# Kernel optimization log

Hardware: AMD Instinct MI355X
Metric: run time of the kernel (lower is better)

## Reference

```python
import jax, jax.numpy as jnp
import numpy as np

B, N, D, H = 64, 196, 768, 3072
QMAX = 127.0  # 8-bit symmetric: clamp to [-128, 127]


def ste_round(x):
    # straight-through-estimator round (QAT)
    return x + jax.lax.stop_gradient(jnp.round(x) - x)


def q_linear_diag(x, w, b, a_sf):
    """Quantized diagonal linear (ResMLP Affine / LayerScale as QuantLinear)."""
    w_sf = jnp.max(jnp.abs(w)) / QMAX            # per-tensor weight scale
    w_int = ste_round(w / w_sf)                  # int8 weights (|.|<=127)
    out_int = (x / a_sf) * w_int
    if b is not None:
        out_int = out_int + ste_round(b / (a_sf * w_sf))  # 32-bit bias
    return out_int * (a_sf * w_sf), w_sf


def q_linear_dense(x, w, b, a_sf):
    """Quantized dense linear: int8 GEMM + int32 bias, dequant with a_sf*w_sf."""
    w_sf = jnp.max(jnp.abs(w)) / QMAX
    w_int = jnp.clip(ste_round(w / w_sf), -QMAX - 1, QMAX)
    out_int = jnp.einsum('...i,oi->...o', x / a_sf, w_int) + ste_round(b / (a_sf * w_sf))
    return out_int * (a_sf * w_sf), w_sf


def q_act(x, pre_sf, new_sf, identity=None, id_sf=None):
    """HAWQ-style QuantAct: fixed-point requantization to scale new_sf (8-bit)."""
    if identity is None:
        z_int = ste_round(x / pre_sf)
        out_int = ste_round(z_int * (pre_sf / new_sf))
    else:
        # main branch (x - identity) requantized with pre_sf, identity with id_sf
        z_int = ste_round((x - identity) / pre_sf)
        out_int = ste_round(z_int * (pre_sf / new_sf)) \
                + ste_round(ste_round(identity / id_sf) * (id_sf / new_sf))
    out_int = jnp.clip(out_int, -QMAX - 1, QMAX)
    return out_int * new_sf, new_sf


def _forward(x, norm1_w, norm1_b, attn_w, attn_b, gamma1_w,
             norm2_w, norm2_b, fc1_w, fc1_b, fc2_w, fc2_b, gamma2_w, act_sfs):
    a_sf = act_sfs[0]
    # --- token-mixing half ---
    identity, id_sf = x, a_sf
    x, w_sf = q_linear_diag(x, norm1_w, norm1_b, a_sf)         # norm1 (affine)
    x = jnp.swapaxes(x, 1, 2)                                  # [B, D, N]
    x, a_sf = q_act(x, a_sf * w_sf, act_sfs[1])                # quant_act1
    x, w_sf = q_linear_dense(x, attn_w, attn_b, a_sf)          # attn (cross-patch)
    x = jnp.swapaxes(x, 1, 2)                                  # [B, N, D]
    x, a_sf = q_act(x, a_sf * w_sf, act_sfs[2])                # quant_act2
    x, w_sf = q_linear_diag(x, gamma1_w, None, a_sf)           # gamma_1 (layerscale)
    x = x + identity
    x, a_sf = q_act(x, a_sf * w_sf, act_sfs[3], identity, id_sf)  # quant_act_int32_1
    # --- MLP half ---
    identity, id_sf = x, a_sf
    x, w_sf = q_linear_diag(x, norm2_w, norm2_b, a_sf)         # norm2
    x, a_sf = q_act(x, a_sf * w_sf, act_sfs[4])                # quant_act3
    x, w_sf = q_linear_dense(x, fc1_w, fc1_b, a_sf)            # mlp.fc1
    x = jax.nn.relu(x)
    x, a_sf = q_act(x, a_sf * w_sf, act_sfs[5])                # mlp.quant_act1
    x, w_sf = q_linear_dense(x, fc2_w, fc2_b, a_sf)            # mlp.fc2
    x, a_sf = q_act(x, a_sf * w_sf, act_sfs[6])                # mlp.quant_act2
    x, w_sf = q_linear_diag(x, gamma2_w, None, a_sf)           # gamma_2
    x = x + identity
    x, a_sf = q_act(x, a_sf * w_sf, act_sfs[7], identity, id_sf)  # quant_act_int32_2
    return x, a_sf


def setup_inputs() -> dict:
    key = jax.random.key(0)
    ks = jax.random.split(key, 16)
    act_sfs = jax.random.uniform(ks[14], (8,), jnp.float32, 0.02, 0.06)
    x = jax.random.normal(ks[0], (B, N, D), jnp.float32)
    # input is already quantized at scale act_sfs[0]
    x = jnp.clip(jnp.round(x / act_sfs[0]), -128, 127) * act_sfs[0]
    s = 0.05
    return {
        'x': x,
        'norm1_w': 1.0 + s * jax.random.normal(ks[1], (D,), jnp.float32),
        'norm1_b': s * jax.random.normal(ks[2], (D,), jnp.float32),
        'attn_w': jax.random.normal(ks[3], (N, N), jnp.float32) / np.sqrt(N),
        'attn_b': s * jax.random.normal(ks[4], (N,), jnp.float32),
        'gamma1_w': 0.1 + s * jax.random.normal(ks[5], (D,), jnp.float32),
        'norm2_w': 1.0 + s * jax.random.normal(ks[6], (D,), jnp.float32),
        'norm2_b': s * jax.random.normal(ks[7], (D,), jnp.float32),
        'fc1_w': jax.random.normal(ks[8], (H, D), jnp.float32) / np.sqrt(D),
        'fc1_b': s * jax.random.normal(ks[9], (H,), jnp.float32),
        'fc2_w': jax.random.normal(ks[10], (D, H), jnp.float32) / np.sqrt(H),
        'fc2_b': s * jax.random.normal(ks[11], (D,), jnp.float32),
        'gamma2_w': 0.1 + s * jax.random.normal(ks[12], (D,), jnp.float32),
        'act_sfs': act_sfs,
    }


def reference(x, norm1_w, norm1_b, attn_w, attn_b, gamma1_w,
              norm2_w, norm2_b, fc1_w, fc1_b, fc2_w, fc2_b, gamma2_w, act_sfs):
    return _forward(x, norm1_w, norm1_b, attn_w, attn_b, gamma1_w,
                    norm2_w, norm2_b, fc1_w, fc1_b, fc2_w, fc2_b, gamma2_w, act_sfs)
```

## Files before the change

kernel.cpp:

```cpp
#include <hip/hip_runtime.h>

#define B_ 64
#define N_ 196
#define D_ 768
#define H_ 3072
#define M_ (B_*N_)
#define NP 256

typedef int int4v __attribute__((ext_vector_type(4)));
typedef signed char i8;

#define WS_MAX 0
#define WS_W1F 16
#define WS_B1F (16+768)
#define WS_G1F (16+768*2)
#define WS_W2F (16+768*3)
#define WS_B2F (16+768*4)
#define WS_G2F (16+768*5)
#define WS_BA  (16+768*6)
#define WS_BF1 (WS_BA+256)
#define WS_BF2 (WS_BF1+3072)
#define OFF_WA   40960ull
#define OFF_FC1  (OFF_WA+65536ull)
#define OFF_FC2  (OFF_FC1+2359296ull)
#define OFF_X2   (OFF_FC2+2359296ull)
#define OFF_Q3   (OFF_X2+9633792ull)
#define OFF_Q4   (OFF_Q3+9633792ull)
#define OFF_Q1T  OFF_Q4

__device__ __forceinline__ float clamp8(float v){ return fminf(fmaxf(v,-128.f),127.f); }

__device__ __forceinline__ void async16(const void* g, void* l){
    __builtin_amdgcn_global_load_lds((const __attribute__((address_space(1))) void*)g,
                                     (__attribute__((address_space(3))) void*)l, 16, 0, 0);
}

__global__ void k_init(char* ws, const float* __restrict__ act, float* out_tail){
    int id = blockIdx.x*256 + threadIdx.x;
    if (blockIdx.x == 0){
        float* f = (float*)ws;
        if (threadIdx.x < 8) f[WS_MAX+threadIdx.x] = 0.f;
        if (threadIdx.x == 8) *out_tail = act[7];
    }
    if (id < 4096){ int4v z = {0,0,0,0}; ((int4v*)(ws+OFF_WA))[id] = z; }
}

__global__ void k_maxabs(const float* __restrict__ p0, const float* __restrict__ p1,
                         const float* __restrict__ p2, const float* __restrict__ p3,
                         const float* __restrict__ p4, const float* __restrict__ p5,
                         const float* __restrict__ p6, float* wsmax){
    const float* ps[7] = {p0,p1,p2,p3,p4,p5,p6};
    const int    n4s[7] = {192, 9604, 192, 192, 589824, 589824, 192};
    int tid = blockIdx.y;
    const float4* p = (const float4*)ps[tid]; int n4 = n4s[tid];
    float m = 0.f;
    for (int i = blockIdx.x*blockDim.x + threadIdx.x; i < n4; i += gridDim.x*blockDim.x){
        float4 v = p[i];
        m = fmaxf(m, fmaxf(fmaxf(fabsf(v.x),fabsf(v.y)), fmaxf(fabsf(v.z),fabsf(v.w))));
    }
    #pragma unroll
    for (int off = 32; off; off >>= 1) m = fmaxf(m, __shfl_down(m, off, 64));
    __shared__ float red[4];
    int lane = threadIdx.x & 63, wv = threadIdx.x >> 6;
    if (lane == 0) red[wv] = m;
    __syncthreads();
    if (threadIdx.x == 0){
        float mm = red[0];
        for (int w = 1; w < (int)blockDim.x/64; w++) mm = fmaxf(mm, red[w]);
        atomicMax((unsigned*)&wsmax[tid], __float_as_uint(mm));
    }
}

__device__ __forceinline__ size_t frag_off(int o, int k, int K){
    int g = o >> 4, c = k >> 6;
    int lane = (o & 15) + (((k >> 4) & 3) << 4);
    return (((size_t)g*(K>>6) + c)*64 + lane)*16 + (k & 15);
}

__global__ void k_qweights(const float* __restrict__ n1w, const float* __restrict__ n1b,
                           const float* __restrict__ aw,  const float* __restrict__ ab,
                           const float* __restrict__ g1w, const float* __restrict__ n2w,
                           const float* __restrict__ n2b, const float* __restrict__ f1w,
                           const float* __restrict__ f1b, const float* __restrict__ f2w,
                           const float* __restrict__ f2b, const float* __restrict__ g2w,
                           const float* __restrict__ act, char* ws){
    float* fws = (float*)ws;
    int*   iws = (int*)ws;
    const float* mx = fws + WS_MAX;
    long i = (long)blockIdx.x*blockDim.x + threadIdx.x;
    const long F4 = 589824;
    if (i < F4){ float sf = mx[4]/127.0f;
        float4 v = ((const float4*)f1w)[i];
        int o = (int)(i/192), kb = (int)(i%192)*4;
        unsigned b0 = (unsigned)(unsigned char)(i8)(int)fminf(fmaxf(rintf(v.x/sf),-128.f),127.f);
        unsigned b1 = (unsigned)(unsigned char)(i8)(int)fminf(fmaxf(rintf(v.y/sf),-128.f),127.f);
        unsigned b2 = (unsigned)(unsigned char)(i8)(int)fminf(fmaxf(rintf(v.z/sf),-128.f),127.f);
        unsigned b3 = (unsigned)(unsigned char)(i8)(int)fminf(fmaxf(rintf(v.w/sf),-128.f),127.f);
        *(unsigned*)(ws + OFF_FC1 + frag_off(o, kb, 768)) = b0 | (b1<<8) | (b2<<16) | (b3<<24);
        return; }
    i -= F4;
    if (i < F4){ float sf = mx[5]/127.0f;
        float4 v = ((const float4*)f2w)[i];
        int o = (int)(i/768), kb = (int)(i%768)*4;
        unsigned b0 = (unsigned)(unsigned char)(i8)(int)fminf(fmaxf(rintf(v.x/sf),-128.f),127.f);
        unsigned b1 = (unsigned)(unsigned char)(i8)(int)fminf(fmaxf(rintf(v.y/sf),-128.f),127.f);
        unsigned b2 = (unsigned)(unsigned char)(i8)(int)fminf(fmaxf(rintf(v.z/sf),-128.f),127.f);
        unsigned b3 = (unsigned)(unsigned char)(i8)(int)fminf(fmaxf(rintf(v.w/sf),-128.f),127.f);
        *(unsigned*)(ws + OFF_FC2 + frag_off(o, kb, 3072)) = b0 | (b1<<8) | (b2<<16) | (b3<<24);
        return; }
    i -= F4;
    if (i < 38416){ float sf = mx[1]/127.0f;
        int o = (int)(i/196), k = (int)(i%196);
        ((i8*)(ws+OFF_WA))[frag_off(o, k, NP)] =
            (i8)(int)fminf(fmaxf(rintf(aw[i]/sf),-128.f),127.f); return; }
    i -= 38416;
    if (i < 768){ float sf = mx[0]/127.0f; fws[WS_W1F+i] = rintf(n1w[i]/sf); return; }
    i -= 768;
    if (i < 768){ float sf = mx[0]/127.0f; fws[WS_B1F+i] = rintf(n1b[i]/(act[0]*sf)); return; }
    i -= 768;
    if (i < 768){ float sf = mx[2]/127.0f; fws[WS_G1F+i] = rintf(g1w[i]/sf); return; }
    i -= 768;
    if (i < 768){ float sf = mx[3]/127.0f; fws[WS_W2F+i] = rintf(n2w[i]/sf); return; }
    i -= 768;
    if (i < 768){ float sf = mx[3]/127.0f; fws[WS_B2F+i] = rintf(n2b[i]/(act[3]*sf)); return; }
    i -= 768;
    if (i < 768){ float sf = mx[6]/127.0f; fws[WS_G2F+i] = rintf(g2w[i]/sf); return; }
    i -= 768;
    if (i < 196){ float sf = mx[1]/127.0f; iws[WS_BA+i] = (int)rintf(ab[i]/(act[1]*sf)); return; }
    i -= 196;
    if (i < 3072){ float sf = mx[4]/127.0f; iws[WS_BF1+i] = (int)rintf(f1b[i]/(act[4]*sf)); return; }
    i -= 3072;
    if (i < 768){ float sf = mx[5]/127.0f; iws[WS_BF2+i] = (int)rintf(f2b[i]/(act[5]*sf)); return; }
}

__global__ __launch_bounds__(256) void k_stage1(const float* __restrict__ x,
                                                const char* __restrict__ wsc,
                                                char* __restrict__ ws,
                                                const float* __restrict__ act){
    __shared__ i8 T[64][80];
    const float* fws = (const float*)wsc;
    int b = blockIdx.z, n0 = blockIdx.y*64, d0 = blockIdx.x*64;
    int t = threadIdx.x;
    float a0 = act[0];
    float w1sf = fws[WS_MAX+0]/127.0f;
    float r1 = (a0*w1sf)/act[1];
    int dl = (t & 15) * 4;
    int d  = d0 + dl;
    float4 wv = *(const float4*)(fws + WS_W1F + d);
    float4 bv = *(const float4*)(fws + WS_B1F + d);
    #pragma unroll
    for (int pass = 0; pass < 4; pass++){
        int nl = (t >> 4) + pass*16;
        int n  = n0 + nl;
        i8 q[4] = {0,0,0,0};
        if (n < 196){
            float4 xv = *(const float4*)(x + ((size_t)b*196 + n)*768 + d);
            float o0 = rintf(xv.x/a0*wv.x + bv.x);
            float o1 = rintf(xv.y/a0*wv.y + bv.y);
            float o2 = rintf(xv.z/a0*wv.z + bv.z);
            float o3 = rintf(xv.w/a0*wv.w + bv.w);
            q[0] = (i8)(int)clamp8(rintf(o0*r1));
            q[1] = (i8)(int)clamp8(rintf(o1*r1));
            q[2] = (i8)(int)clamp8(rintf(o2*r1));
            q[3] = (i8)(int)clamp8(rintf(o3*r1));
        }
        T[dl+0][nl] = q[0]; T[dl+1][nl] = q[1];
        T[dl+2][nl] = q[2]; T[dl+3][nl] = q[3];
    }
    __syncthreads();
    i8* q1T = (i8*)(ws + OFF_Q1T) + (size_t)b*(48*4*1024);
    int gl = t >> 6, lane = t & 63;
    int d_loc = gl*16 + (lane & 15);
    int n16   = ((lane >> 4) & 3) * 16;
    int4v v = *(const int4v*)&T[d_loc][n16];
    size_t dst = (((size_t)((d0>>4)+gl)*4 + (n0>>6))*64 + lane)*16;
    *(int4v*)(q1T + dst) = v;
}

__device__ __forceinline__ void gemm_i8_bd(const i8* __restrict__ qa, const i8* __restrict__ wbF,
                                           size_t lda, int n0, int K, int4v acc[4][4],
                                           i8* As, int t){
    int lane = t & 63;
    int w = t >> 6, wm = w & 1, wn = w >> 1;
    int lr = lane >> 2, lc = lane & 3;
    const i8* ga = qa + (size_t)(w*32 + lr)*lda + lc*16;
    int loff = (w*32 + lr)*64 + lc*16;
    int kc = K >> 6;
    size_t ntS = (size_t)kc*1024;
    const i8* gb = wbF + ((size_t)((n0>>4) + wn*4))*ntS + lane*16;
    int arow = (wm*64 + (lane&15))*64 + (lane>>4)*16;
    int4v a[4], b0[4], b1[4];
    async16(ga,          As + loff);
    async16(ga + 16*lda, As + loff + 16*64);
    #pragma unroll
    for (int nt=0;nt<4;nt++) b0[nt] = *(const int4v*)(gb + nt*ntS);
    for (int i = 0; i < kc; i += 2){
        __syncthreads();
        if (i+1 < kc){
            async16(ga + (i+1)*64,          As + 8192 + loff);
            async16(ga + (i+1)*64 + 16*lda, As + 8192 + loff + 16*64);
            #pragma unroll
            for (int nt=0;nt<4;nt++) b1[nt] = *(const int4v*)(gb + (i+1)*1024 + nt*ntS);
        }
        #pragma unroll
        for (int mt=0;mt<4;mt++) a[mt] = *(const int4v*)(As + arow + mt*1024);
        #pragma unroll
        for (int mt=0;mt<4;mt++)
            #pragma unroll
            for (int nt=0;nt<4;nt++)
                acc[mt][nt] = __builtin_amdgcn_mfma_i32_16x16x64_i8(a[mt], b0[nt], acc[mt][nt],0,0,0);
        __syncthreads();
        if (i+2 < kc){
            async16(ga + (i+2)*64,          As + loff);
            async16(ga + (i+2)*64 + 16*lda, As + loff + 16*64);
            #pragma unroll
            for (int nt=0;nt<4;nt++) b0[nt] = *(const int4v*)(gb + (i+2)*1024 + nt*ntS);
        }
        #pragma unroll
        for (int mt=0;mt<4;mt++) a[mt] = *(const int4v*)(As + 8192 + arow + mt*1024);
        #pragma unroll
        for (int mt=0;mt<4;mt++)
            #pragma unroll
            for (int nt=0;nt<4;nt++)
                acc[mt][nt] = __builtin_amdgcn_mfma_i32_16x16x64_i8(a[mt], b1[nt], acc[mt][nt],0,0,0);
    }
}

__global__ __launch_bounds__(256) void k_attn(const char* __restrict__ ws,
                                              const float* __restrict__ x,
                                              const float* __restrict__ act){
    __shared__ char smem[32768];
    const float* fws = (const float*)ws;
    const int*   iws = (const int*)ws;
    int b = blockIdx.z;
    int m0 = blockIdx.x*128, n0 = blockIdx.y*128;
    int t = threadIdx.x, lane = t & 63;
    int wm = (t>>6)&1, wn = t>>7;
    const i8* pa = (const i8*)(ws + OFF_WA)  + ((size_t)((m0>>4)+wm*4)*4)*1024 + lane*16;
    const i8* pb = (const i8*)(ws + OFF_Q1T) + (size_t)b*(48*4*1024)
                   + ((size_t)((n0>>4)+wn*4)*4)*1024 + lane*16;
    int4v acc[4][4]; int4v zz = {0,0,0,0};
    #pragma unroll
    for (int mt=0;mt<4;mt++) for (int nt=0;nt<4;nt++) acc[mt][nt] = zz;
    int4v a0[4], b0[4], a1[4], b1[4];
    #pragma unroll
    for (int mt=0;mt<4;mt++) a0[mt] = *(const int4v*)(pa + mt*4096);
    #pragma unroll
    for (int nt=0;nt<4;nt++) b0[nt] = *(const int4v*)(pb + nt*4096);
    for (int c = 0; c < 4; c += 2){
        #pragma unroll
        for (int mt=0;mt<4;mt++) a1[mt] = *(const int4v*)(pa + (c+1)*1024 + mt*4096);
        #pragma unroll
        for (int nt=0;nt<4;nt++) b1[nt] = *(const int4v*)(pb + (c+1)*1024 + nt*4096);
        #pragma unroll
        for (int mt=0;mt<4;mt++)
            #pragma unroll
            for (int nt=0;nt<4;nt++)
                acc[mt][nt] = __builtin_amdgcn_mfma_i32_16x16x64_i8(a0[mt], b0[nt], acc[mt][nt],0,0,0);
        if (c+2 < 4){
            #pragma unroll
            for (int mt=0;mt<4;mt++) a0[mt] = *(const int4v*)(pa + (c+2)*1024 + mt*4096);
            #pragma unroll
            for (int nt=0;nt<4;nt++) b0[nt] = *(const int4v*)(pb + (c+2)*1024 + nt*4096);
        }
        #pragma unroll
        for (int mt=0;mt<4;mt++)
            #pragma unroll
            for (int nt=0;nt<4;nt++)
                acc[mt][nt] = __builtin_amdgcn_mfma_i32_16x16x64_i8(a1[mt], b1[nt], acc[mt][nt],0,0,0);
    }

    float a0s=act[0], a1s=act[1], a2=act[2], a3=act[3], a4=act[4];
    float wasf = fws[WS_MAX+1]/127.0f; float r2  = (a1s*wasf)/a2;
    float g1sf = fws[WS_MAX+2]/127.0f; float r3a = (a2*g1sf)/a3; float r3b = a0s/a3;
    float w2sf = fws[WS_MAX+3]/127.0f; float r4  = (a3*w2sf)/a4;
    float g1v[4], w2v[4], b2v[4];
    #pragma unroll
    for (int nt=0;nt<4;nt++){
        int d = n0 + wn*64 + nt*16 + (lane&15);
        g1v[nt] = fws[WS_G1F + d]; w2v[nt] = fws[WS_W2F + d]; b2v[nt] = fws[WS_B2F + d];
    }
    i8* Xs = (i8*)smem;
    i8* Qs = (i8*)smem + 16384;
    i8* x2 = (i8*)(ws + OFF_X2);
    i8* q3 = (i8*)(ws + OFF_Q3);
    #pragma unroll
    for (int mt=0;mt<4;mt++){
        #pragma unroll
        for (int r=0;r<4;r++){
            int ml = wm*64 + mt*16 + (lane>>4)*4 + r;
            int o  = m0 + ml;
            int ba = iws[WS_BA + o];
            #pragma unroll
            for (int nt=0;nt<4;nt++){
                int nl = wn*64 + nt*16 + (lane&15);
                int d  = n0 + nl;
                float s2 = (float)(acc[mt][nt][r] + ba);
                float q2 = clamp8(rintf(s2*r2));
                float o3v = q2*g1v[nt];
                float xv = (o < 196) ? x[((size_t)b*196 + o)*768 + d] : 0.f;
                float idi = rintf(xv/a0s);
                float tt = rintf(o3v*r3a) + rintf(idi*r3b);
                tt = clamp8(tt);
                float o4 = tt*w2v[nt] + b2v[nt];
                float qr = clamp8(rintf(o4*r4));
                Xs[ml*128 + nl] = (i8)(int)tt;
                Qs[ml*128 + nl] = (i8)(int)qr;
            }
        }
    }
    __syncthreads();
    #pragma unroll
    for (int e=0;e<4;e++){
        int id = t + e*256;
        int row = id>>3, c = id&7;
        int o = m0 + row;
        if (o < 196){
            size_t g = ((size_t)b*196 + o)*768 + n0 + c*16;
            *(int4v*)(x2 + g) = *(const int4v*)(Xs + row*128 + c*16);
            *(int4v*)(q3 + g) = *(const int4v*)(Qs + row*128 + c*16);
        }
    }
}

__global__ __launch_bounds__(256) void k_fc1(const char* __restrict__ ws, const float* __restrict__ act){
    __shared__ char smem[16384];
    const float* fws = (const float*)ws;
    const int*   iws = (const int*)ws;
    int m0 = blockIdx.x*128, n0 = blockIdx.y*128;
    const i8* qa = (const i8*)(ws+OFF_Q3) + (size_t)m0*768;
    const i8* wb = (const i8*)(ws+OFF_FC1);
    const int* bias = iws + WS_BF1;
    i8* qout = (i8*)(ws+OFF_Q4);
    int t = threadIdx.x, lane = t & 63;
    int wm = (t>>6)&1, wn = t>>7;
    int4v acc[4][4]; int4v zz = {0,0,0,0};
    #pragma unroll
    for (int mt=0;mt<4;mt++) for (int nt=0;nt<4;nt++) acc[mt][nt] = zz;
    gemm_i8_bd(qa, wb, 768, n0, 768, acc, (i8*)smem, t);
    float wsf = fws[WS_MAX+4]/127.0f;
    float r5 = (act[4]*wsf)/act[5];
    int bcol[4];
    #pragma unroll
    for (int nt=0;nt<4;nt++) bcol[nt] = bias[n0 + wn*64 + nt*16 + (lane&15)];
    __syncthreads();
    i8* Cs = (i8*)smem;
    #pragma unroll
    for (int mt=0;mt<4;mt++){
        #pragma unroll
        for (int nt=0;nt<4;nt++){
            int nl = wn*64 + nt*16 + (lane&15);
            #pragma unroll
            for (int r=0;r<4;r++){
                int s = acc[mt][nt][r] + bcol[nt];
                if (s < 0) s = 0;
                float q = clamp8(rintf((float)s * r5));
                int ml = wm*64 + mt*16 + (lane>>4)*4 + r;
                Cs[ml*128 + nl] = (i8)(int)q;
            }
        }
    }
    __syncthreads();
    #pragma unroll
    for (int e=0;e<4;e++){
        int id2 = t + e*256;
        int row = id2>>3, c = id2&7;
        *(int4v*)(qout + (size_t)(m0+row)*3072 + n0 + c*16) = *(const int4v*)(Cs + row*128 + c*16);
    }
}

__global__ __launch_bounds__(256) void k_fc2(const char* __restrict__ ws, const float* __restrict__ act,
                                             float* __restrict__ out){
    __shared__ char smem[16384];
    const float* fws = (const float*)ws;
    const int*   iws = (const int*)ws;
    int m0 = blockIdx.x*128, n0 = blockIdx.y*128;
    const i8* qa = (const i8*)(ws+OFF_Q4) + (size_t)m0*3072;
    const i8* wb = (const i8*)(ws+OFF_FC2);
    const int* bias = iws + WS_BF2;
    const float* g2f = fws + WS_G2F;
    const i8* x2 = (const i8*)(ws+OFF_X2);
    int t = threadIdx.x, lane = t & 63;
    int wm = (t>>6)&1, wn = t>>7;
    int4v acc[4][4]; int4v zz = {0,0,0,0};
    #pragma unroll
    for (int mt=0;mt<4;mt++) for (int nt=0;nt<4;nt++) acc[mt][nt] = zz;
    gemm_i8_bd(qa, wb, 3072, n0, 3072, acc, (i8*)smem, t);
    float a3=act[3], a5=act[5], a6=act[6], a7=act[7];
    float wsf  = fws[WS_MAX+5]/127.0f; float r6  = (a5*wsf)/a6;
    float g2sf = fws[WS_MAX+6]/127.0f; float r7a = (a6*g2sf)/a7; float r7b = a3/a7;
    int bcol[4]; float g2v[4];
    #pragma unroll
    for (int nt=0;nt<4;nt++){
        int nc = n0 + wn*64 + nt*16 + (lane&15);
        bcol[nt] = bias[nc]; g2v[nt] = g2f[nc];
    }
    #pragma unroll
    for (int mt=0;mt<4;mt++){
        #pragma unroll
        for (int nt=0;nt<4;nt++){
            int nc = n0 + wn*64 + nt*16 + (lane&15);
            #pragma unroll
            for (int r=0;r<4;r++){
                int ml = wm*64 + mt*16 + (lane>>4)*4 + r;
                size_t gi = (size_t)(m0+ml)*768 + nc;
                int s = acc[mt][nt][r] + bcol[nt];
                float q6 = clamp8(rintf((float)s*r6));
                float o7 = q6*g2v[nt];
                float idi = (float)x2[gi];
                float tt = rintf(o7*r7a) + rintf(idi*r7b);
                tt = clamp8(tt);
                out[gi] = tt*a7;
            }
        }
    }
}

extern "C" void kernel_launch(void* const* d_in, const int* in_sizes, int n_in,
                              void* d_out, int out_size, void* d_ws, size_t ws_size,
                              hipStream_t stream){
    const float* x   = (const float*)d_in[0];
    const float* n1w = (const float*)d_in[1];
    const float* n1b = (const float*)d_in[2];
    const float* aw  = (const float*)d_in[3];
    const float* ab  = (const float*)d_in[4];
    const float* g1w = (const float*)d_in[5];
    const float* n2w = (const float*)d_in[6];
    const float* n2b = (const float*)d_in[7];
    const float* f1w = (const float*)d_in[8];
    const float* f1b = (const float*)d_in[9];
    const float* f2w = (const float*)d_in[10];
    const float* f2b = (const float*)d_in[11];
    const float* g2w = (const float*)d_in[12];
    const float* act = (const float*)d_in[13];
    char* ws = (char*)d_ws;
    float* out = (float*)d_out;

    k_init<<<16,256,0,stream>>>(ws, act, out + (size_t)B_*N_*D_);
    k_maxabs<<<dim3(120,7),256,0,stream>>>(n1w, aw, g1w, n2w, f1w, f2w, g2w, (float*)ws);
    long qwThreads = 2L*589824 + 38416 + 768L*6 + 196 + 3072 + 768;
    k_qweights<<<(int)((qwThreads+255)/256),256,0,stream>>>(n1w,n1b,aw,ab,g1w,n2w,n2b,
                                                            f1w,f1b,f2w,f2b,g2w,act,ws);
    k_stage1<<<dim3(12,4,64),256,0,stream>>>(x, ws, ws, act);
    k_attn<<<dim3(2,6,64),256,0,stream>>>(ws, x, act);
    k_fc1<<<dim3(98,24),256,0,stream>>>(ws, act);
    k_fc2<<<dim3(98,6),256,0,stream>>>(ws, act, out);
}
```

Baseline: 299.4 us.

## Store fc1/fc2 activations in MFMA fragment layout and load directly to registers

The producer kernels (attn epilogue and fc1 epilogue) now write the quantized activations Q3 and Q4 in a pre-tiled MFMA fragment order instead of row-major. This lets fc1 and fc2 read both A and B operands straight from global memory into registers with a shared double-buffered helper, removing the LDS staging, async global-to-LDS copies and the per-step barriers. The trade-off is no LDS reuse of A tiles across waves, so each wave fetches its own A fragments from global/L2, and the epilogue scatter writes are more complex.

```diff
diff --git a/kernel.cpp b/kernel.cpp
--- a/kernel.cpp
+++ b/kernel.cpp
@@ -29,11 +29,6 @@
 #define OFF_Q1T  OFF_Q4
 
 __device__ __forceinline__ float clamp8(float v){ return fminf(fmaxf(v,-128.f),127.f); }
-
-__device__ __forceinline__ void async16(const void* g, void* l){
-    __builtin_amdgcn_global_load_lds((const __attribute__((address_space(1))) void*)g,
-                                     (__attribute__((address_space(3))) void*)l, 16, 0, 0);
-}
 
 __global__ void k_init(char* ws, const float* __restrict__ act, float* out_tail){
     int id = blockIdx.x*256 + threadIdx.x;
@@ -177,52 +172,35 @@
     *(int4v*)(q1T + dst) = v;
 }
 
-__device__ __forceinline__ void gemm_i8_bd(const i8* __restrict__ qa, const i8* __restrict__ wbF,
-                                           size_t lda, int n0, int K, int4v acc[4][4],
-                                           i8* As, int t){
-    int lane = t & 63;
-    int w = t >> 6, wm = w & 1, wn = w >> 1;
-    int lr = lane >> 2, lc = lane & 3;
-    const i8* ga = qa + (size_t)(w*32 + lr)*lda + lc*16;
-    int loff = (w*32 + lr)*64 + lc*16;
-    int kc = K >> 6;
-    size_t ntS = (size_t)kc*1024;
-    const i8* gb = wbF + ((size_t)((n0>>4) + wn*4))*ntS + lane*16;
-    int arow = (wm*64 + (lane&15))*64 + (lane>>4)*16;
-    int4v a[4], b0[4], b1[4];
-    async16(ga,          As + loff);
-    async16(ga + 16*lda, As + loff + 16*64);
-    #pragma unroll
-    for (int nt=0;nt<4;nt++) b0[nt] = *(const int4v*)(gb + nt*ntS);
-    for (int i = 0; i < kc; i += 2){
-        __syncthreads();
-        if (i+1 < kc){
-            async16(ga + (i+1)*64,          As + 8192 + loff);
-            async16(ga + (i+1)*64 + 16*lda, As + 8192 + loff + 16*64);
-            #pragma unroll
-            for (int nt=0;nt<4;nt++) b1[nt] = *(const int4v*)(gb + (i+1)*1024 + nt*ntS);
-        }
-        #pragma unroll
-        for (int mt=0;mt<4;mt++) a[mt] = *(const int4v*)(As + arow + mt*1024);
+__device__ __forceinline__ void gemm_i8_direct_frag(const i8* pa, const i8* pb,
+                                                    int KC, size_t sA, size_t sB,
+                                                    int4v acc[4][4]){
+    int4v a0[4], b0[4], a1[4], b1[4];
+    #pragma unroll
+    for (int mt=0;mt<4;mt++) a0[mt] = *(const int4v*)(pa + mt*sA);
+    #pragma unroll
+    for (int nt=0;nt<4;nt++) b0[nt] = *(const int4v*)(pb + nt*sB);
+    for (int c = 0; c < KC; c += 2){
+        #pragma unroll
+        for (int mt=0;mt<4;mt++) a1[mt] = *(const int4v*)(pa + (c+1)*1024 + mt*sA);
+        #pragma unroll
+        for (int nt=0;nt<4;nt++) b1[nt] = *(const int4v*)(pb + (c+1)*1024 + nt*sB);
         #pragma unroll
         for (int mt=0;mt<4;mt++)
             #pragma unroll
             for (int nt=0;nt<4;nt++)
-                acc[mt][nt] = __builtin_amdgcn_mfma_i32_16x16x64_i8(a[mt], b0[nt], acc[mt][nt],0,0,0);
-        __syncthreads();
-        if (i+2 < kc){
-            async16(ga + (i+2)*64,          As + loff);
-            async16(ga + (i+2)*64 + 16*lda, As + loff + 16*64);
-            #pragma unroll
-            for (int nt=0;nt<4;nt++) b0[nt] = *(const int4v*)(gb + (i+2)*1024 + nt*ntS);
-        }
-        #pragma unroll
-        for (int mt=0;mt<4;mt++) a[mt] = *(const int4v*)(As + 8192 + arow + mt*1024);
+                acc[mt][nt] = __builtin_amdgcn_mfma_i32_16x16x64_i8(a0[mt], b0[nt], acc[mt][nt],0,0,0);
+        if (c+2 < KC){
+            #pragma unroll
+            for (int mt=0;mt<4;mt++) a0[mt] = *(const int4v*)(pa + (c+2)*1024 + mt*sA);
+            #pragma unroll
+            for (int nt=0;nt<4;nt++) b0[nt] = *(const int4v*)(pb + (c+2)*1024 + nt*sB);
+        }
         #pragma unroll
         for (int mt=0;mt<4;mt++)
             #pragma unroll
             for (int nt=0;nt<4;nt++)
-                acc[mt][nt] = __builtin_amdgcn_mfma_i32_16x16x64_i8(a[mt], b1[nt], acc[mt][nt],0,0,0);
+                acc[mt][nt] = __builtin_amdgcn_mfma_i32_16x16x64_i8(a1[mt], b1[nt], acc[mt][nt],0,0,0);
     }
 }
 
@@ -242,33 +220,7 @@
     int4v acc[4][4]; int4v zz = {0,0,0,0};
     #pragma unroll
     for (int mt=0;mt<4;mt++) for (int nt=0;nt<4;nt++) acc[mt][nt] = zz;
-    int4v a0[4], b0[4], a1[4], b1[4];
-    #pragma unroll
-    for (int mt=0;mt<4;mt++) a0[mt] = *(const int4v*)(pa + mt*4096);
-    #pragma unroll
-    for (int nt=0;nt<4;nt++) b0[nt] = *(const int4v*)(pb + nt*4096);
-    for (int c = 0; c < 4; c += 2){
-        #pragma unroll
-        for (int mt=0;mt<4;mt++) a1[mt] = *(const int4v*)(pa + (c+1)*1024 + mt*4096);
-        #pragma unroll
-        for (int nt=0;nt<4;nt++) b1[nt] = *(const int4v*)(pb + (c+1)*1024 + nt*4096);
-        #pragma unroll
-        for (int mt=0;mt<4;mt++)
-            #pragma unroll
-            for (int nt=0;nt<4;nt++)
-                acc[mt][nt] = __builtin_amdgcn_mfma_i32_16x16x64_i8(a0[mt], b0[nt], acc[mt][nt],0,0,0);
-        if (c+2 < 4){
-            #pragma unroll
-            for (int mt=0;mt<4;mt++) a0[mt] = *(const int4v*)(pa + (c+2)*1024 + mt*4096);
-            #pragma unroll
-            for (int nt=0;nt<4;nt++) b0[nt] = *(const int4v*)(pb + (c+2)*1024 + nt*4096);
-        }
-        #pragma unroll
-        for (int mt=0;mt<4;mt++)
-            #pragma unroll
-            for (int nt=0;nt<4;nt++)
-                acc[mt][nt] = __builtin_amdgcn_mfma_i32_16x16x64_i8(a1[mt], b1[nt], acc[mt][nt],0,0,0);
-    }
+    gemm_i8_direct_frag(pa, pb, 4, 4096, 4096, acc);
 
     float a0s=act[0], a1s=act[1], a2=act[2], a3=act[3], a4=act[4];
     float wasf = fws[WS_MAX+1]/127.0f; float r2  = (a1s*wasf)/a2;
@@ -282,8 +234,8 @@
     }
     i8* Xs = (i8*)smem;
     i8* Qs = (i8*)smem + 16384;
-    i8* x2 = (i8*)(ws + OFF_X2);
-    i8* q3 = (i8*)(ws + OFF_Q3);
+    i8* x2  = (i8*)(ws + OFF_X2);
+    i8* q3F = (i8*)(ws + OFF_Q3);
     #pragma unroll
     for (int mt=0;mt<4;mt++){
         #pragma unroll
@@ -318,7 +270,11 @@
         if (o < 196){
             size_t g = ((size_t)b*196 + o)*768 + n0 + c*16;
             *(int4v*)(x2 + g) = *(const int4v*)(Xs + row*128 + c*16);
-            *(int4v*)(q3 + g) = *(const int4v*)(Qs + row*128 + c*16);
+            int r2i = b*196 + o;
+            int lane_d = (r2i & 15) + ((c & 3) << 4);
+            size_t dst = (((size_t)(r2i>>4))*12 + (size_t)(n0>>6) + (c>>2))*1024
+                         + (size_t)lane_d*16;
+            *(int4v*)(q3F + dst) = *(const int4v*)(Qs + row*128 + c*16);
         }
     }
 }
@@ -328,22 +284,21 @@
     const float* fws = (const float*)ws;
     const int*   iws = (const int*)ws;
     int m0 = blockIdx.x*128, n0 = blockIdx.y*128;
-    const i8* qa = (const i8*)(ws+OFF_Q3) + (size_t)m0*768;
-    const i8* wb = (const i8*)(ws+OFF_FC1);
-    const int* bias = iws + WS_BF1;
-    i8* qout = (i8*)(ws+OFF_Q4);
     int t = threadIdx.x, lane = t & 63;
     int wm = (t>>6)&1, wn = t>>7;
+    const i8* pa = (const i8*)(ws+OFF_Q3)  + ((size_t)(m0>>4) + wm*4)*(12*1024) + (size_t)lane*16;
+    const i8* pb = (const i8*)(ws+OFF_FC1) + ((size_t)(n0>>4) + wn*4)*(12*1024) + (size_t)lane*16;
+    const int* bias = iws + WS_BF1;
+    i8* q4F = (i8*)(ws+OFF_Q4);
     int4v acc[4][4]; int4v zz = {0,0,0,0};
     #pragma unroll
     for (int mt=0;mt<4;mt++) for (int nt=0;nt<4;nt++) acc[mt][nt] = zz;
-    gemm_i8_bd(qa, wb, 768, n0, 768, acc, (i8*)smem, t);
+    gemm_i8_direct_frag(pa, pb, 12, 12*1024, 12*1024, acc);
     float wsf = fws[WS_MAX+4]/127.0f;
     float r5 = (act[4]*wsf)/act[5];
     int bcol[4];
     #pragma unroll
     for (int nt=0;nt<4;nt++) bcol[nt] = bias[n0 + wn*64 + nt*16 + (lane&15)];
-    __syncthreads();
     i8* Cs = (i8*)smem;
     #pragma unroll
     for (int mt=0;mt<4;mt++){
@@ -363,29 +318,34 @@
     __syncthreads();
     #pragma unroll
     for (int e=0;e<4;e++){
-        int id2 = t + e*256;
-        int row = id2>>3, c = id2&7;
-        *(int4v*)(qout + (size_t)(m0+row)*3072 + n0 + c*16) = *(const int4v*)(Cs + row*128 + c*16);
+        int id = t + e*256;
+        int mg  = id >> 7;
+        int kc2 = (id >> 6) & 1;
+        int ld  = id & 63;
+        int row = mg*16 + (ld & 15);
+        int cb  = kc2*64 + ((ld>>4)&3)*16;
+        int4v v = *(const int4v*)(Cs + row*128 + cb);
+        size_t dst = (((size_t)(m0>>4) + mg)*48 + (size_t)(n0>>6) + kc2)*1024 + (size_t)ld*16;
+        *(int4v*)(q4F + dst) = v;
     }
 }
 
 __global__ __launch_bounds__(256) void k_fc2(const char* __restrict__ ws, const float* __restrict__ act,
                                              float* __restrict__ out){
-    __shared__ char smem[16384];
     const float* fws = (const float*)ws;
     const int*   iws = (const int*)ws;
     int m0 = blockIdx.x*128, n0 = blockIdx.y*128;
-    const i8* qa = (const i8*)(ws+OFF_Q4) + (size_t)m0*3072;
-    const i8* wb = (const i8*)(ws+OFF_FC2);
+    int t = threadIdx.x, lane = t & 63;
+    int wm = (t>>6)&1, wn = t>>7;
+    const i8* pa = (const i8*)(ws+OFF_Q4)  + ((size_t)(m0>>4) + wm*4)*(48*1024) + (size_t)lane*16;
+    const i8* pb = (const i8*)(ws+OFF_FC2) + ((size_t)(n0>>4) + wn*4)*(48*1024) + (size_t)lane*16;
     const int* bias = iws + WS_BF2;
     const float* g2f = fws + WS_G2F;
     const i8* x2 = (const i8*)(ws+OFF_X2);
-    int t = threadIdx.x, lane = t & 63;
-    int wm = (t>>6)&1, wn = t>>7;
     int4v acc[4][4]; int4v zz = {0,0,0,0};
     #pragma unroll
     for (int mt=0;mt<4;mt++) for (int nt=0;nt<4;nt++) acc[mt][nt] = zz;
-    gemm_i8_bd(qa, wb, 3072, n0, 3072, acc, (i8*)smem, t);
+    gemm_i8_direct_frag(pa, pb, 48, 48*1024, 48*1024, acc);
     float a3=act[3], a5=act[5], a6=act[6], a7=act[7];
     float wsf  = fws[WS_MAX+5]/127.0f; float r6  = (a5*wsf)/a6;
     float g2sf = fws[WS_MAX+6]/127.0f; float r7a = (a6*g2sf)/a7; float r7b = a3/a7;
```

After: 335.3 us. 12.0% more time.
